# Kernel optimization log

Measured on AMD Instinct MI355X. Metric: run time of the kernel, lower is better.

## Reference

```python
import jax, jax.numpy as jnp
import numpy as np

B, T, F = 2048, 128, 128
H, L, K = 512, 8, 10  # hidden_dim, levels, conv_size
CHUNK = H // L
GATES = 4 * H + 2 * L


def setup_inputs() -> dict:
    key = jax.random.key(0)
    ks = jax.random.split(key, 12)
    s_k = 1.0 / np.sqrt(F + 1)
    s_r = 1.0 / np.sqrt(H + 1)
    s_s = 1.0 / np.sqrt(H)
    s_rs = 1.0 / np.sqrt(H // 6)
    s_c = 1.0 / np.sqrt(H * K)
    return {
        'x': jax.random.normal(ks[0], (B, T, F), jnp.float32),
        'time': jax.random.uniform(ks[1], (B, T), jnp.float32),
        'Wk': jax.random.normal(ks[2], (F + 1, GATES), jnp.float32) * s_k,
        'bk': jnp.zeros((GATES,), jnp.float32),
        'Wr': jax.random.normal(ks[3], (H + 1, GATES), jnp.float32) * s_r,
        'br': jnp.zeros((GATES,), jnp.float32),
        'Ws': jax.random.normal(ks[4], (H, H // 6), jnp.float32) * s_s,
        'bs': jax.random.normal(ks[5], (H // 6,), jnp.float32) * 0.01,
        'Wrs': jax.random.normal(ks[6], (H // 6, H), jnp.float32) * s_rs,
        'brs': jax.random.normal(ks[7], (H,), jnp.float32) * 0.01,
        'conv_w': jax.random.normal(ks[8], (H, H, K), jnp.float32) * s_c,  # [out_ch, in_ch, k]
        'conv_b': jax.random.normal(ks[9], (H,), jnp.float32) * 0.01,
    }


def _cumax_l2r(z):
    return jnp.cumsum(jax.nn.softmax(z, axis=-1), axis=-1)


def _cumax_r2l(z):
    return jnp.flip(jnp.cumsum(jax.nn.softmax(jnp.flip(z, -1), axis=-1), axis=-1), -1)


def _phase_forward(x, time, Wk, bk, Wr, br, Ws, bs, Wrs, brs, conv_w, conv_b):
    def step(carry, xs):
        c, h, tmp_h, tmp_dis = carry
        xt, dt = xs
        dt = dt[:, None]
        xo = (jnp.concatenate([xt, dt], -1) @ Wk + bk
              + jnp.concatenate([h, dt], -1) @ Wr + br)  # [B, 4H+2L]
        fm = _cumax_l2r(xo[:, :L])[:, :, None]        # [B, L, 1]
        im = _cumax_r2l(xo[:, L:2 * L])[:, :, None]   # [B, L, 1]
        g = xo[:, 2 * L:].reshape(-1, 4 * L, CHUNK)
        f = jax.nn.sigmoid(g[:, :L])
        i = jax.nn.sigmoid(g[:, L:2 * L])
        o = jax.nn.sigmoid(g[:, 2 * L:3 * L])
        c_in = jnp.tanh(g[:, 3 * L:])
        c_last = c.reshape(-1, L, CHUNK)
        ov = fm * im
        c_new = ov * (f * c_last + i * c_in) + (fm - ov) * c_last + (im - ov) * c_in
        h_new = (o * jnp.tanh(c_new)).reshape(-1, H)
        dist = 1.0 - jnp.mean(fm[..., 0], axis=-1)   # [B]
        tmp_h = jnp.concatenate([tmp_h[1:], h_new[None]], 0)
        tmp_dis = jnp.concatenate([tmp_dis[1:], dist[None]], 0)
        return (c_new.reshape(-1, H), h_new, tmp_h, tmp_dis), dist

    init = (jnp.zeros((B, H), x.dtype), jnp.zeros((B, H), x.dtype),
            jnp.zeros((K, B, H), x.dtype), jnp.zeros((K, B), x.dtype))
    (_, _, tmp_h, tmp_dis), distance = jax.lax.scan(
        step, init, (jnp.transpose(x, (1, 0, 2)), time.T))

    local_dis = jax.nn.softmax(jnp.cumsum(tmp_dis.T, axis=1), axis=1)   # [B, K]
    local_h = jnp.transpose(tmp_h, (1, 2, 0)) * local_dis[:, None, :]   # [B, H, K]
    theme = jax.nn.sigmoid(
        jnp.maximum(jnp.mean(local_h, axis=-1) @ Ws + bs, 0.0) @ Wrs + brs)  # [B, H]
    conv_out = jnp.einsum('bhk,ohk->bo', local_h, conv_w) + conv_b      # valid conv, out len 1
    return theme * conv_out, distance


def reference(x, time, Wk, bk, Wr, br, Ws, bs, Wrs, brs, conv_w, conv_b):
    return _phase_forward(x, time, Wk, bk, Wr, br, Ws, bs, Wrs, brs, conv_w, conv_b)
```

## Files before the change

### kernel.cpp

```cpp
#include <hip/hip_runtime.h>
#include <hip/hip_bf16.h>
#include <cstddef>
#include <cstdint>

namespace {

constexpr int B = 2048, T = 128, F = 128, H = 512, L = 8, KW = 10;
constexpr int GATES = 2064;
constexpr int NG = 2048;
constexpr int KIN = 640;
constexpr int HS = 85;
constexpr int RC = H * KW;
constexpr int KS = 8;
constexpr int NROW = 144;

constexpr int ABUF = 0;
constexpr int BRES = 16384;
constexpr int BROT = 126976;
constexpr int DTSO = 154624;
constexpr int SMEM_SZ = 155136;

typedef __attribute__((ext_vector_type(8))) short short8;
typedef __attribute__((ext_vector_type(4))) float f32x4;
typedef unsigned long long ull;

__device__ __forceinline__ float fsigmoid_(float x) {
    return __builtin_amdgcn_rcpf(1.0f + __expf(-x));
}
__device__ __forceinline__ float ftanh_(float x) {
    return 1.0f - 2.0f * __builtin_amdgcn_rcpf(1.0f + __expf(2.0f * x));
}

__device__ __forceinline__ void gl_lds16(const void* g, void* l) {
    __builtin_amdgcn_global_load_lds(
        (const __attribute__((address_space(1))) unsigned int*)g,
        (__attribute__((address_space(3))) unsigned int*)l,
        16, 0, 0);
}

__device__ __forceinline__ ull h_atomic_load(const void* p) {
    return __hip_atomic_load((const ull*)p, __ATOMIC_RELAXED, __HIP_MEMORY_SCOPE_AGENT);
}

__global__ __launch_bounds__(256) void prep_wgt(
    const float* __restrict__ Wk, const float* __restrict__ Wr,
    __hip_bfloat16* __restrict__ WgT)
{
    __shared__ float tile[64 * 65];
    const int tid = threadIdx.x;
    const int c0 = blockIdx.x * 64, k0 = blockIdx.y * 64;
#pragma unroll
    for (int rep = 0; rep < 16; ++rep) {
        int e = rep * 256 + tid;
        int kl = e >> 6, cl = e & 63;
        int col = c0 + cl;
        int nt = col >> 7, cc = col & 127;
        int n = 16 + ((cc >> 4) & 3) * 512 + nt * 32 + ((cc >> 6) & 1) * 16 + (cc & 15);
        int k = k0 + kl;
        tile[kl * 65 + cl] = (k < F) ? Wk[(size_t)k * GATES + n] : Wr[(size_t)(k - F) * GATES + n];
    }
    __syncthreads();
    const int cl = tid >> 2, q = tid & 3;
    unsigned short buf[16];
#pragma unroll
    for (int i = 0; i < 16; ++i) {
        float f = tile[(q * 16 + i) * 65 + cl];
        __hip_bfloat16 bv = __float2bfloat16(f);
        buf[i] = *(unsigned short*)&bv;
    }
    int col = c0 + cl;
    int nt = col >> 7, rin = col & 127;
    unsigned short* dst = (unsigned short*)WgT + (size_t)nt * NROW * KIN + (size_t)rin * KIN + k0 + q * 16;
    *(short8*)dst = *(short8*)&buf[0];
    *(short8*)(dst + 8) = *(short8*)&buf[8];
}

__global__ void prep_w16rep(const float* __restrict__ Wk, const float* __restrict__ Wr,
                            __hip_bfloat16* __restrict__ WgT)
{
    int idx = blockIdx.x * blockDim.x + threadIdx.x;
    if (idx >= 16 * 16 * KIN) return;
    int nt = idx / (16 * KIN);
    int rem = idx % (16 * KIN);
    int n = rem / KIN, k = rem % KIN;
    float v = (k < F) ? Wk[(size_t)k * GATES + n] : Wr[(size_t)(k - F) * GATES + n];
    WgT[(size_t)nt * NROW * KIN + (size_t)(128 + n) * KIN + k] = __float2bfloat16(v);
}

__global__ void prep_small(const float* __restrict__ Wk, const float* __restrict__ bk,
                           const float* __restrict__ Wr, const float* __restrict__ br,
                           float* __restrict__ biasg, float* __restrict__ wrowg,
                           float* __restrict__ bias16, float* __restrict__ wrow16)
{
    const int total = 2 * NG + 32;
    for (int idx = threadIdx.x; idx < total; idx += 256) {
        if (idx < NG) {
            int col = idx;
            int nt = col >> 7, cc = col & 127;
            int n = 16 + ((cc >> 4) & 3) * 512 + nt * 32 + ((cc >> 6) & 1) * 16 + (cc & 15);
            biasg[col] = bk[n] + br[n];
        } else if (idx < 2 * NG) {
            int col = idx - NG;
            int nt = col >> 7, cc = col & 127;
            int n = 16 + ((cc >> 4) & 3) * 512 + nt * 32 + ((cc >> 6) & 1) * 16 + (cc & 15);
            wrowg[col] = Wk[(size_t)F * GATES + n] + Wr[(size_t)H * GATES + n];
        } else if (idx < 2 * NG + 16) {
            int n = idx - 2 * NG;
            bias16[n] = bk[n] + br[n];
        } else {
            int n = idx - 2 * NG - 16;
            wrow16[n] = Wk[(size_t)F * GATES + n] + Wr[(size_t)H * GATES + n];
        }
    }
}

__global__ void convert_x(const float* __restrict__ x, __hip_bfloat16* __restrict__ xb) {
    int i = blockIdx.x * blockDim.x + threadIdx.x;
    size_t o = (size_t)i * 4;
    if (o >= (size_t)B * T * F) return;
    float4 v = *(const float4*)(x + o);
    xb[o + 0] = __float2bfloat16(v.x);
    xb[o + 1] = __float2bfloat16(v.y);
    xb[o + 2] = __float2bfloat16(v.z);
    xb[o + 3] = __float2bfloat16(v.w);
}

__global__ void prep_convw(const float* __restrict__ conv_w, __hip_bfloat16* __restrict__ CWb) {
    int i = blockIdx.x * blockDim.x + threadIdx.x;
    if (i >= H * RC / 4) return;
    size_t o = (size_t)i * 4;
    float4 v = *(const float4*)(conv_w + o);
    CWb[o + 0] = __float2bfloat16(v.x);
    CWb[o + 1] = __float2bfloat16(v.y);
    CWb[o + 2] = __float2bfloat16(v.z);
    CWb[o + 3] = __float2bfloat16(v.w);
}

__global__ __launch_bounds__(256) void prep_tmet(const float* __restrict__ tin,
                                                 float* __restrict__ tout)
{
    __shared__ float tl[32][33];
    const int bb = blockIdx.x * 32, tt = blockIdx.y * 32;
    const int tx = threadIdx.x & 31, ty = threadIdx.x >> 5;
#pragma unroll
    for (int r = 0; r < 32; r += 8)
        tl[ty + r][tx] = tin[(size_t)(bb + ty + r) * T + tt + tx];
    __syncthreads();
#pragma unroll
    for (int r = 0; r < 32; r += 8)
        tout[(size_t)(tt + ty + r) * B + bb + tx] = tl[tx][ty + r];
}

struct StepArgs {
    const __hip_bfloat16* xb;
    __hip_bfloat16* h0;
    __hip_bfloat16* h1;
    const __hip_bfloat16* WgT;
    const float* biasg;
    const float* wrowg;
    const float* bias16;
    const float* wrow16;
    const float* tmeT;
    __hip_bfloat16* tmp_h;
    float* tmp_ds;
    float* dist_out;
    unsigned* bar;
};

__global__ __launch_bounds__(512, 2) void persistent_step(StepArgs a)
{
    __shared__ __align__(16) char smem[SMEM_SZ];
    float* logitS = (float*)smem;
    float* fmimS = (float*)(smem + BROT);
    unsigned short* hstageS = (unsigned short*)(smem + 135168);
    float* dts = (float*)(smem + DTSO);

    const int tid = threadIdx.x;
    const int wave = tid >> 6;
    const int wr = wave >> 1, wc = wave & 1;
    const int quad = (tid & 63) >> 4, m16 = tid & 15;
    const int l = blockIdx.x;
    const int nt = ((l & 7) << 1) | ((l >> 3) & 1);
    const int mt = l >> 4;
    const int m0 = mt * 128;

    const int o0 = tid * 16;
    const int arow = o0 >> 6;
    const int asl = ((((o0 >> 4) & 3) ^ ((arow >> 1) & 3)) << 3);
    const char* xbT = (const char*)a.xb + (size_t)(m0 + arow) * (T * F * 2) + asl * 2;
    const size_t hbyte = (size_t)(m0 + arow) * (H * 2) + asl * 2;
    const unsigned short* wgt_tile = (const unsigned short*)a.WgT + (size_t)nt * NROW * KIN;
    const int brow0 = o0 >> 6;
    const int bsl0 = ((((o0 >> 4) & 3) ^ ((brow0 >> 1) & 3)) << 3);
    const char* bsT0 = (const char*)(wgt_tile + (size_t)brow0 * KIN + bsl0);
    const int ob1 = 8192 + tid * 16;
    const int brow1 = ob1 >> 6;
    const int bsl1 = ((((ob1 >> 4) & 3) ^ ((brow1 >> 1) & 3)) << 3);
    const char* bsT1 = (const char*)(wgt_tile + (size_t)brow1 * KIN + bsl1);
    const bool bv1 = (tid < 64);

    auto stageB = [&](int s, int bufbyte) {
        gl_lds16(bsT0 + s * 64, smem + bufbyte + o0);
        if (bv1) gl_lds16(bsT1 + s * 64, smem + bufbyte + ob1);
    };

    const int hcol = nt * 32 + wc * 16 + m16;
    const int lidx = hcol >> 6;
    float bj[4], wj[4];
#pragma unroll
    for (int j = 0; j < 4; ++j) {
        int col = nt * 128 + wc * 64 + j * 16 + m16;
        bj[j] = a.biasg[col];
        wj[j] = a.wrowg[col];
    }
    float b16r[16], w16r[16];
#pragma unroll
    for (int n = 0; n < 16; ++n) { b16r[n] = a.bias16[n]; w16r[n] = a.wrow16[n]; }

    const unsigned short* Abase = (const unsigned short*)smem;

    float creg[2][4] = {};
    ull areg[2][2];

    {
#pragma unroll
        for (int s = 0; s < 12; ++s) stageB(s, BRES + s * 9216);
        gl_lds16(xbT, smem + o0);
        stageB(12, BROT + 0 * 9216);
        stageB(13, BROT + 1 * 9216);
        areg[1][0] = h_atomic_load(xbT + 64);  areg[1][1] = h_atomic_load(xbT + 72);
        areg[0][0] = h_atomic_load(xbT + 128); areg[0][1] = h_atomic_load(xbT + 136);
    }
    __syncthreads();

#pragma unroll 1
    for (int t = 0; t < T; ++t) {
        const char* xt = xbT + (size_t)t * 256;
        const char* hs = (const char*)((t & 1) ? a.h1 : a.h0) + hbyte;
        unsigned* hout32 = (unsigned*)((t & 1) ? a.h0 : a.h1);

        if (tid < 128) dts[tid] = a.tmeT[(size_t)t * B + m0 + tid];

        f32x4 acc[2][4] = {};
        f32x4 acc16[2] = {};

#pragma unroll
        for (int ki = 0; ki < 20; ++ki) {
            if (ki > 0) {
                if (ki <= 13) {
                    asm volatile("s_waitcnt lgkmcnt(0)" ::: "memory");
                } else if (ki <= 17) {
                    if (bv1) asm volatile("s_waitcnt vmcnt(6) lgkmcnt(0)" ::: "memory");
                    else     asm volatile("s_waitcnt vmcnt(5) lgkmcnt(0)" ::: "memory");
                } else if (ki == 18) {
                    if (bv1) asm volatile("s_waitcnt vmcnt(4) lgkmcnt(0)" ::: "memory");
                    else     asm volatile("s_waitcnt vmcnt(3) lgkmcnt(0)" ::: "memory");
                } else {
                    asm volatile("s_waitcnt vmcnt(0) lgkmcnt(0)" ::: "memory");
                }
                __builtin_amdgcn_s_barrier();
                __builtin_amdgcn_sched_barrier(0);
            }
            const int nxt = ki + 1;
            if (nxt < 20) {
                char* adst = smem + (nxt & 1) * 8192 + o0;
                *(ull*)adst = areg[nxt & 1][0];
                *(ull*)(adst + 8) = areg[nxt & 1][1];
            }
            if (ki >= 12 && ki <= 17) {
                const int s = ki + 2;
                stageB(s, BROT + ((s - 12) % 3) * 9216);
            }
            __builtin_amdgcn_sched_barrier(0);
            const int fut = ki + 3;
            if (fut < 20) {
                if (fut <= 3) {
                    areg[fut & 1][0] = h_atomic_load(xt + fut * 64);
                    areg[fut & 1][1] = h_atomic_load(xt + fut * 64 + 8);
                } else {
                    areg[fut & 1][0] = h_atomic_load(hs + fut * 64 - 256);
                    areg[fut & 1][1] = h_atomic_load(hs + fut * 64 - 248);
                }
            }
            __builtin_amdgcn_sched_barrier(0);
            const unsigned short* A = Abase + (ki & 1) * 4096;
            const unsigned short* Bb = (const unsigned short*)
                (smem + (ki < 12 ? BRES + ki * 9216 : BROT + ((ki - 12) % 3) * 9216));
            short8 av[2], bv[4];
#pragma unroll
            for (int i = 0; i < 2; ++i) {
                int ar = wr * 32 + i * 16 + m16;
                av[i] = *(const short8*)&A[ar * 32 + ((quad ^ ((ar >> 1) & 3)) << 3)];
            }
#pragma unroll
            for (int j = 0; j < 4; ++j) {
                int br = wc * 64 + j * 16 + m16;
                bv[j] = *(const short8*)&Bb[br * 32 + ((quad ^ ((br >> 1) & 3)) << 3)];
            }
#pragma unroll
            for (int i = 0; i < 2; ++i)
#pragma unroll
                for (int j = 0; j < 4; ++j)
                    acc[i][j] = __builtin_amdgcn_mfma_f32_16x16x32_bf16(av[i], bv[j], acc[i][j], 0, 0, 0);
            if (wc == 0) {
                int lr = 128 + m16;
                short8 wv = *(const short8*)&Bb[lr * 32 + ((quad ^ ((lr >> 1) & 3)) << 3)];
                acc16[0] = __builtin_amdgcn_mfma_f32_16x16x32_bf16(av[0], wv, acc16[0], 0, 0, 0);
                acc16[1] = __builtin_amdgcn_mfma_f32_16x16x32_bf16(av[1], wv, acc16[1], 0, 0, 0);
            }
        }
        __syncthreads();

        if (wc == 0) {
#pragma unroll
            for (int i = 0; i < 2; ++i)
#pragma unroll
                for (int r = 0; r < 4; ++r)
                    logitS[(wr * 32 + i * 16 + quad * 4 + r) * 17 + m16] = acc16[i][r];
        }
        __syncthreads();

        if (tid < 256) {
            const int row = tid & 127;
            const int m = m0 + row;
            const bool hi = tid >= 128;
            const float dt = dts[row];
            const int off = hi ? 8 : 0;
            float z[8];
#pragma unroll
            for (int n = 0; n < 8; ++n)
                z[n] = logitS[row * 17 + off + n] + b16r[off + n] + dt * w16r[off + n];
            float mx = z[0];
#pragma unroll
            for (int j = 1; j < 8; ++j) mx = fmaxf(mx, z[j]);
            float e[8], s = 0.f;
#pragma unroll
            for (int j = 0; j < 8; ++j) { e[j] = __expf(z[j] - mx); s += e[j]; }
            const float inv = __builtin_amdgcn_rcpf(s);
            if (!hi) {
                float run = 0.f, fsum = 0.f;
#pragma unroll
                for (int j = 0; j < 8; ++j) { run += e[j]; float fmv = run * inv; fmimS[row * 16 + j] = fmv; fsum += fmv; }
                if (nt == 0) {
                    float d = 1.0f - fsum * 0.125f;
                    a.dist_out[(size_t)t * B + m] = d;
                    if (t >= T - KW) a.tmp_ds[(size_t)(t - (T - KW)) * B + m] = d;
                }
            } else {
                float run = 0.f;
#pragma unroll
                for (int j = 7; j >= 0; --j) { run += e[j]; fmimS[row * 16 + 8 + j] = run * inv; }
            }
        }
        __syncthreads();

#pragma unroll
        for (int i = 0; i < 2; ++i) {
#pragma unroll
            for (int r = 0; r < 4; ++r) {
                int rl = wr * 32 + i * 16 + quad * 4 + r;
                int m = m0 + rl;
                float dt = dts[rl];
                float fmv = fmimS[rl * 16 + lidx];
                float imv = fmimS[rl * 16 + 8 + lidx];
                float fg = fsigmoid_(acc[i][0][r] + bj[0] + dt * wj[0]);
                float ig = fsigmoid_(acc[i][1][r] + bj[1] + dt * wj[1]);
                float og = fsigmoid_(acc[i][2][r] + bj[2] + dt * wj[2]);
                float ci = ftanh_(acc[i][3][r] + bj[3] + dt * wj[3]);
                float ov = fmv * imv;
                float cl = creg[i][r];
                float cn = ov * (fg * cl + ig * ci) + (fmv - ov) * cl + (imv - ov) * ci;
                float hn = og * ftanh_(cn);
                creg[i][r] = cn;
                __hip_bfloat16 hb = __float2bfloat16(hn);
                hstageS[rl * 32 + (wc * 16 + m16)] = *(unsigned short*)&hb;
                if (t >= T - KW) a.tmp_h[((size_t)(t - (T - KW)) * B + m) * H + hcol] = hb;
            }
        }
        __syncthreads();

        {
            const unsigned* hs32 = (const unsigned*)hstageS;
#pragma unroll
            for (int wds = 0; wds < 4; ++wds) {
                int wi = wds * 512 + tid;
                int row = wi >> 4, cp = wi & 15;
                unsigned v = hs32[row * 16 + cp];
                __hip_atomic_store(hout32 + (size_t)(m0 + row) * (H / 2) + nt * 16 + cp, v,
                                   __ATOMIC_RELAXED, __HIP_MEMORY_SCOPE_AGENT);
            }
        }

        __syncthreads();
        if (t != T - 1) {
            const char* xn = xbT + (size_t)(t + 1) * 256;
            gl_lds16(xn, smem + o0);
            stageB(12, BROT + 0 * 9216);
            stageB(13, BROT + 1 * 9216);
            areg[1][0] = h_atomic_load(xn + 64);  areg[1][1] = h_atomic_load(xn + 72);
            areg[0][0] = h_atomic_load(xn + 128); areg[0][1] = h_atomic_load(xn + 136);
            if (tid == 0) {
                unsigned* ctr = a.bar + (mt << 6);
                __hip_atomic_fetch_add(ctr, 1u, __ATOMIC_RELAXED, __HIP_MEMORY_SCOPE_AGENT);
                const unsigned tgt = 16u * (unsigned)(t + 1);
                for (int it = 0; it < (1 << 22); ++it) {
                    if (__hip_atomic_load(ctr, __ATOMIC_RELAXED, __HIP_MEMORY_SCOPE_AGENT) >= tgt) break;
                    __builtin_amdgcn_s_sleep(2);
                }
            }
            __syncthreads();
        }
    }
}

__global__ __launch_bounds__(128) void post_local(
    const __hip_bfloat16* __restrict__ tmp_h, const float* __restrict__ tmp_dis,
    float* __restrict__ mean_h, __hip_bfloat16* __restrict__ Ahk)
{
    const int b = blockIdx.x;
    const int tid = threadIdx.x;
    __shared__ float ld[KW];
    if (tid == 0) {
        float cd[KW];
        float run = 0.f;
        for (int k = 0; k < KW; ++k) { run += tmp_dis[(size_t)k * B + b]; cd[k] = run; }
        float mx = cd[0];
        for (int k = 1; k < KW; ++k) mx = fmaxf(mx, cd[k]);
        float s = 0.f;
        for (int k = 0; k < KW; ++k) { cd[k] = expf(cd[k] - mx); s += cd[k]; }
        for (int k = 0; k < KW; ++k) ld[k] = cd[k] / s;
    }
    __syncthreads();
    float ldr[KW];
#pragma unroll
    for (int k = 0; k < KW; ++k) ldr[k] = ld[k];
    for (int h = tid; h < H; h += 128) {
        float s = 0.f;
#pragma unroll
        for (int k = 0; k < KW; ++k) {
            float v = __bfloat162float(tmp_h[((size_t)k * B + b) * H + h]) * ldr[k];
            s += v;
            Ahk[(size_t)b * RC + h * KW + k] = __float2bfloat16(v);
        }
        mean_h[(size_t)b * H + h] = s * (1.0f / KW);
    }
}

__global__ void theme1_k(const float* __restrict__ mean_h, const float* __restrict__ Ws,
                         const float* __restrict__ bs, float* __restrict__ t1)
{
    int idx = blockIdx.x * blockDim.x + threadIdx.x;
    if (idx >= B * HS) return;
    int b = idx / HS, j = idx % HS;
    float s = bs[j];
    const float* mh = mean_h + (size_t)b * H;
    for (int h = 0; h < H; ++h) s += mh[h] * Ws[(size_t)h * HS + j];
    t1[idx] = fmaxf(s, 0.f);
}

__global__ void theme2_k(const float* __restrict__ t1, const float* __restrict__ Wrs,
                         const float* __restrict__ brs, float* __restrict__ theme)
{
    int idx = blockIdx.x * blockDim.x + threadIdx.x;
    if (idx >= B * H) return;
    int b = idx / H, o = idx % H;
    float s = brs[o];
    const float* tv = t1 + (size_t)b * HS;
    for (int j = 0; j < HS; ++j) s += tv[j] * Wrs[(size_t)j * H + o];
    theme[idx] = 1.0f / (1.0f + expf(-s));
}

__global__ __launch_bounds__(256) void conv_split(
    const __hip_bfloat16* __restrict__ Ahk, const __hip_bfloat16* __restrict__ CWb,
    float* __restrict__ Pbuf)
{
    __shared__ __align__(16) unsigned short As2[128 * 64];
    __shared__ __align__(16) unsigned short Bs2[128 * 64];
    const int tid = threadIdx.x;
    const int wave = tid >> 6;
    const int wr = wave >> 1, wc = wave & 1;
    const int quad = (tid & 63) >> 4, m16 = tid & 15;
    const int n0 = blockIdx.x * 128, m0 = blockIdx.y * 128;
    const int ksb = blockIdx.z * (RC / KS);

    f32x4 acc[4][4] = {};
    for (int k0 = 0; k0 < RC / KS; k0 += 64) {
#pragma unroll
        for (int p = 0; p < 4; ++p) {
            int o = p * 4096 + tid * 16;
            int row = o >> 7, slot = (o >> 4) & 7;
            int kg = ksb + k0 + (slot ^ (row & 7)) * 8;
            gl_lds16((const unsigned short*)Ahk + (size_t)(m0 + row) * RC + kg, (char*)As2 + o);
            gl_lds16((const unsigned short*)CWb + (size_t)(n0 + row) * RC + kg, (char*)Bs2 + o);
        }
        __syncthreads();
#pragma unroll
        for (int c2 = 0; c2 < 2; ++c2) {
            const int k8 = c2 * 4 + quad;
            short8 av[4], bv[4];
#pragma unroll
            for (int i = 0; i < 4; ++i) {
                int arow = wr * 64 + i * 16 + m16;
                av[i] = *(const short8*)&As2[arow * 64 + (k8 ^ (arow & 7)) * 8];
            }
#pragma unroll
            for (int j = 0; j < 4; ++j) {
                int brow = wc * 64 + j * 16 + m16;
                bv[j] = *(const short8*)&Bs2[brow * 64 + (k8 ^ (brow & 7)) * 8];
            }
#pragma unroll
            for (int i = 0; i < 4; ++i)
#pragma unroll
                for (int j = 0; j < 4; ++j)
                    acc[i][j] = __builtin_amdgcn_mfma_f32_16x16x32_bf16(av[i], bv[j], acc[i][j], 0, 0, 0);
        }
        __syncthreads();
    }
    float* P = Pbuf + (size_t)blockIdx.z * B * H;
#pragma unroll
    for (int j = 0; j < 4; ++j) {
        const int col = n0 + wc * 64 + j * 16 + m16;
#pragma unroll
        for (int i = 0; i < 4; ++i) {
            const int rb = m0 + wr * 64 + i * 16 + quad * 4;
#pragma unroll
            for (int r = 0; r < 4; ++r)
                P[(size_t)(rb + r) * H + col] = acc[i][j][r];
        }
    }
}

__global__ void conv_reduce(const float* __restrict__ Pbuf, const float* __restrict__ conv_b,
                            const float* __restrict__ theme, float* __restrict__ out0)
{
    int i = blockIdx.x * blockDim.x + threadIdx.x;
    if (i >= B * H) return;
    float s = conv_b[i & (H - 1)];
#pragma unroll
    for (int ks = 0; ks < KS; ++ks) s += Pbuf[(size_t)ks * B * H + i];
    out0[i] = theme[i] * s;
}

}

extern "C" void kernel_launch(void* const* d_in, const int* in_sizes, int n_in,
                              void* d_out, int out_size, void* d_ws, size_t ws_size,
                              hipStream_t stream)
{
    (void)in_sizes; (void)n_in; (void)out_size; (void)ws_size;
    const float* x      = (const float*)d_in[0];
    const float* tme    = (const float*)d_in[1];
    const float* Wk     = (const float*)d_in[2];
    const float* bk     = (const float*)d_in[3];
    const float* Wr     = (const float*)d_in[4];
    const float* br     = (const float*)d_in[5];
    const float* Ws     = (const float*)d_in[6];
    const float* bs     = (const float*)d_in[7];
    const float* Wrs    = (const float*)d_in[8];
    const float* brs    = (const float*)d_in[9];
    const float* conv_w = (const float*)d_in[10];
    const float* conv_b = (const float*)d_in[11];

    float* out0 = (float*)d_out;
    float* dist_out = out0 + (size_t)B * H;

    char* w = (char*)d_ws;
    __hip_bfloat16* WgT  = (__hip_bfloat16*)w; w += (size_t)16 * NROW * KIN * 2;
    __hip_bfloat16* xb   = (__hip_bfloat16*)w; w += (size_t)B * T * F * 2;
    __hip_bfloat16* CWb  = (__hip_bfloat16*)w; w += (size_t)H * RC * 2;
    __hip_bfloat16* Ahk  = (__hip_bfloat16*)w; w += (size_t)B * RC * 2;
    __hip_bfloat16* hb0  = (__hip_bfloat16*)w; w += (size_t)B * H * 2;
    __hip_bfloat16* hb1  = (__hip_bfloat16*)w; w += (size_t)B * H * 2;
    __hip_bfloat16* tmp_h = (__hip_bfloat16*)w; w += (size_t)KW * B * H * 2;
    float* biasg  = (float*)w; w += (size_t)NG * 4;
    float* wrowg  = (float*)w; w += (size_t)NG * 4;
    float* bias16 = (float*)w; w += 64;
    float* wrow16 = (float*)w; w += 64;
    float* tmp_ds = (float*)w; w += (size_t)KW * B * 4;
    float* mean_h = (float*)w; w += (size_t)B * H * 4;
    float* t1     = (float*)w; w += (size_t)B * HS * 4;
    float* theme  = (float*)w; w += (size_t)B * H * 4;
    float* Pbuf   = (float*)w; w += (size_t)KS * B * H * 4;
    float* tmeT   = (float*)w; w += (size_t)T * B * 4;
    unsigned* bar = (unsigned*)w; w += 4096;

    hipMemsetAsync(hb0, 0, (size_t)B * H * sizeof(__hip_bfloat16), stream);
    hipMemsetAsync(bar, 0, 4096, stream);

    prep_wgt<<<dim3(NG / 64, KIN / 64), 256, 0, stream>>>(Wk, Wr, WgT);
    prep_w16rep<<<(16 * 16 * KIN + 255) / 256, 256, 0, stream>>>(Wk, Wr, WgT);
    prep_small<<<1, 256, 0, stream>>>(Wk, bk, Wr, br, biasg, wrowg, bias16, wrow16);
    convert_x<<<((B * T * F / 4) + 255) / 256, 256, 0, stream>>>(x, xb);
    prep_convw<<<((H * RC / 4) + 255) / 256, 256, 0, stream>>>(conv_w, CWb);
    prep_tmet<<<dim3(B / 32, T / 32), 256, 0, stream>>>(tme, tmeT);

    {
        StepArgs sa;
        sa.xb = xb; sa.h0 = hb0; sa.h1 = hb1; sa.WgT = WgT;
        sa.biasg = biasg; sa.wrowg = wrowg; sa.bias16 = bias16; sa.wrow16 = wrow16;
        sa.tmeT = tmeT; sa.tmp_h = tmp_h; sa.tmp_ds = tmp_ds; sa.dist_out = dist_out;
        sa.bar = bar;
        persistent_step<<<256, 512, 0, stream>>>(sa);
    }

    post_local<<<B, 128, 0, stream>>>(tmp_h, tmp_ds, mean_h, Ahk);
    theme1_k<<<(B * HS + 255) / 256, 256, 0, stream>>>(mean_h, Ws, bs, t1);
    theme2_k<<<(B * H + 255) / 256, 256, 0, stream>>>(t1, Wrs, brs, theme);
    conv_split<<<dim3(H / 128, B / 128, KS), 256, 0, stream>>>(Ahk, CWb, Pbuf);
    conv_reduce<<<(B * H + 255) / 256, 256, 0, stream>>>(Pbuf, conv_b, theme, out0);
}
```

Baseline: 1.771 ms.

## Load A fragments directly into registers and keep 18 B slices resident in LDS

```diff
diff --git a/kernel.cpp b/kernel.cpp
--- a/kernel.cpp
+++ b/kernel.cpp
@@ -14,11 +14,15 @@
 constexpr int KS = 8;
 constexpr int NROW = 144;
 
-constexpr int ABUF = 0;
-constexpr int BRES = 16384;
-constexpr int BROT = 126976;
-constexpr int DTSO = 154624;
-constexpr int SMEM_SZ = 155136;
+constexpr int BSLICE = 8192;
+constexpr int NRES = 18;
+constexpr int RINGA = 147456;
+constexpr int RINGB = 155648;
+constexpr int LOGO  = 147456;
+constexpr int HSTO  = 147456;
+constexpr int DTSO2 = 156160;
+constexpr int FMIMO = 156672;
+constexpr int SMEM_SZ = 163840;
 
 typedef __attribute__((ext_vector_type(8))) short short8;
 typedef __attribute__((ext_vector_type(4))) float f32x4;
@@ -170,10 +174,10 @@
 __global__ __launch_bounds__(512, 2) void persistent_step(StepArgs a)
 {
     __shared__ __align__(16) char smem[SMEM_SZ];
-    float* logitS = (float*)smem;
-    float* fmimS = (float*)(smem + BROT);
-    unsigned short* hstageS = (unsigned short*)(smem + 135168);
-    float* dts = (float*)(smem + DTSO);
+    float* logitS = (float*)(smem + LOGO);
+    float* fmimS  = (float*)(smem + FMIMO);
+    unsigned short* hstageS = (unsigned short*)(smem + HSTO);
+    float* dts = (float*)(smem + DTSO2);
 
     const int tid = threadIdx.x;
     const int wave = tid >> 6;
@@ -183,29 +187,34 @@
     const int nt = ((l & 7) << 1) | ((l >> 3) & 1);
     const int mt = l >> 4;
     const int m0 = mt * 128;
+    const int lidx = nt >> 1;
 
     const int o0 = tid * 16;
-    const int arow = o0 >> 6;
-    const int asl = ((((o0 >> 4) & 3) ^ ((arow >> 1) & 3)) << 3);
-    const char* xbT = (const char*)a.xb + (size_t)(m0 + arow) * (T * F * 2) + asl * 2;
-    const size_t hbyte = (size_t)(m0 + arow) * (H * 2) + asl * 2;
-    const unsigned short* wgt_tile = (const unsigned short*)a.WgT + (size_t)nt * NROW * KIN;
     const int brow0 = o0 >> 6;
     const int bsl0 = ((((o0 >> 4) & 3) ^ ((brow0 >> 1) & 3)) << 3);
+    const unsigned short* wgt_tile = (const unsigned short*)a.WgT + (size_t)nt * NROW * KIN;
     const char* bsT0 = (const char*)(wgt_tile + (size_t)brow0 * KIN + bsl0);
-    const int ob1 = 8192 + tid * 16;
-    const int brow1 = ob1 >> 6;
-    const int bsl1 = ((((ob1 >> 4) & 3) ^ ((brow1 >> 1) & 3)) << 3);
-    const char* bsT1 = (const char*)(wgt_tile + (size_t)brow1 * KIN + bsl1);
-    const bool bv1 = (tid < 64);
-
-    auto stageB = [&](int s, int bufbyte) {
-        gl_lds16(bsT0 + s * 64, smem + bufbyte + o0);
-        if (bv1) gl_lds16(bsT1 + s * 64, smem + bufbyte + ob1);
+    auto stageB = [&](int s, int off) {
+        gl_lds16(bsT0 + s * 64, smem + off + o0);
     };
 
+    const int arow0 = m0 + wr * 32 + m16;
+    const char* xA0 = (const char*)a.xb + (size_t)arow0 * (T * F * 2) + quad * 16;
+    const char* xA1 = xA0 + (size_t)16 * (T * F * 2);
+    const size_t hA0 = (size_t)arow0 * (H * 2) + quad * 16;
+    const size_t hA1 = hA0 + (size_t)16 * (H * 2);
+
+    ull wv20[20][2];
+    if (wc == 0) {
+        const unsigned short* lrow = wgt_tile + (size_t)(128 + m16) * KIN + quad * 8;
+#pragma unroll
+        for (int s = 0; s < 20; ++s) {
+            wv20[s][0] = *(const ull*)(lrow + s * 32);
+            wv20[s][1] = *(const ull*)(lrow + s * 32 + 4);
+        }
+    }
+
     const int hcol = nt * 32 + wc * 16 + m16;
-    const int lidx = hcol >> 6;
     float bj[4], wj[4];
 #pragma unroll
     for (int j = 0; j < 4; ++j) {
@@ -213,104 +222,83 @@
         bj[j] = a.biasg[col];
         wj[j] = a.wrowg[col];
     }
-    float b16r[16], w16r[16];
-#pragma unroll
-    for (int n = 0; n < 16; ++n) { b16r[n] = a.bias16[n]; w16r[n] = a.wrow16[n]; }
-
-    const unsigned short* Abase = (const unsigned short*)smem;
+    const int soff = (tid >= 128 && tid < 256) ? 8 : 0;
+    float b16r8[8], w16r8[8];
+#pragma unroll
+    for (int n = 0; n < 8; ++n) { b16r8[n] = a.bias16[soff + n]; w16r8[n] = a.wrow16[soff + n]; }
 
     float creg[2][4] = {};
-    ull areg[2][2];
+    ull af[3][2][2];
 
     {
 #pragma unroll
-        for (int s = 0; s < 12; ++s) stageB(s, BRES + s * 9216);
-        gl_lds16(xbT, smem + o0);
-        stageB(12, BROT + 0 * 9216);
-        stageB(13, BROT + 1 * 9216);
-        areg[1][0] = h_atomic_load(xbT + 64);  areg[1][1] = h_atomic_load(xbT + 72);
-        areg[0][0] = h_atomic_load(xbT + 128); areg[0][1] = h_atomic_load(xbT + 136);
+        for (int s = 0; s < NRES; ++s) stageB(s, s * BSLICE);
+        stageB(18, RINGA);
+        stageB(19, RINGB);
+        af[0][0][0] = *(const ull*)(xA0);      af[0][0][1] = *(const ull*)(xA0 + 8);
+        af[0][1][0] = *(const ull*)(xA1);      af[0][1][1] = *(const ull*)(xA1 + 8);
+        af[1][0][0] = *(const ull*)(xA0 + 64); af[1][0][1] = *(const ull*)(xA0 + 72);
+        af[1][1][0] = *(const ull*)(xA1 + 64); af[1][1][1] = *(const ull*)(xA1 + 72);
     }
     __syncthreads();
 
 #pragma unroll 1
     for (int t = 0; t < T; ++t) {
-        const char* xt = xbT + (size_t)t * 256;
-        const char* hs = (const char*)((t & 1) ? a.h1 : a.h0) + hbyte;
+        const char* xt0 = xA0 + (size_t)t * 256;
+        const char* xt1 = xA1 + (size_t)t * 256;
+        const char* hbuf = (const char*)((t & 1) ? a.h1 : a.h0);
         unsigned* hout32 = (unsigned*)((t & 1) ? a.h0 : a.h1);
 
-        if (tid < 128) dts[tid] = a.tmeT[(size_t)t * B + m0 + tid];
+        float dtreg = 0.f;
+        if (tid < 128) dtreg = a.tmeT[(size_t)t * B + m0 + tid];
 
         f32x4 acc[2][4] = {};
         f32x4 acc16[2] = {};
 
 #pragma unroll
         for (int ki = 0; ki < 20; ++ki) {
-            if (ki > 0) {
-                if (ki <= 13) {
-                    asm volatile("s_waitcnt lgkmcnt(0)" ::: "memory");
-                } else if (ki <= 17) {
-                    if (bv1) asm volatile("s_waitcnt vmcnt(6) lgkmcnt(0)" ::: "memory");
-                    else     asm volatile("s_waitcnt vmcnt(5) lgkmcnt(0)" ::: "memory");
-                } else if (ki == 18) {
-                    if (bv1) asm volatile("s_waitcnt vmcnt(4) lgkmcnt(0)" ::: "memory");
-                    else     asm volatile("s_waitcnt vmcnt(3) lgkmcnt(0)" ::: "memory");
+            const int ld = ki + 2;
+            if (ld < 20) {
+                const int slot = ld % 3;
+                if (ld <= 3) {
+                    af[slot][0][0] = *(const ull*)(xt0 + ld * 64);
+                    af[slot][0][1] = *(const ull*)(xt0 + ld * 64 + 8);
+                    af[slot][1][0] = *(const ull*)(xt1 + ld * 64);
+                    af[slot][1][1] = *(const ull*)(xt1 + ld * 64 + 8);
                 } else {
-                    asm volatile("s_waitcnt vmcnt(0) lgkmcnt(0)" ::: "memory");
+                    const size_t ko = (size_t)ld * 64 - 256;
+                    af[slot][0][0] = h_atomic_load(hbuf + hA0 + ko);
+                    af[slot][0][1] = h_atomic_load(hbuf + hA0 + ko + 8);
+                    af[slot][1][0] = h_atomic_load(hbuf + hA1 + ko);
+                    af[slot][1][1] = h_atomic_load(hbuf + hA1 + ko + 8);
                 }
-                __builtin_amdgcn_s_barrier();
-                __builtin_amdgcn_sched_barrier(0);
-            }
-            const int nxt = ki + 1;
-            if (nxt < 20) {
-                char* adst = smem + (nxt & 1) * 8192 + o0;
-                *(ull*)adst = areg[nxt & 1][0];
-                *(ull*)(adst + 8) = areg[nxt & 1][1];
-            }
-            if (ki >= 12 && ki <= 17) {
-                const int s = ki + 2;
-                stageB(s, BROT + ((s - 12) % 3) * 9216);
-            }
-            __builtin_amdgcn_sched_barrier(0);
-            const int fut = ki + 3;
-            if (fut < 20) {
-                if (fut <= 3) {
-                    areg[fut & 1][0] = h_atomic_load(xt + fut * 64);
-                    areg[fut & 1][1] = h_atomic_load(xt + fut * 64 + 8);
-                } else {
-                    areg[fut & 1][0] = h_atomic_load(hs + fut * 64 - 256);
-                    areg[fut & 1][1] = h_atomic_load(hs + fut * 64 - 248);
-                }
-            }
-            __builtin_amdgcn_sched_barrier(0);
-            const unsigned short* A = Abase + (ki & 1) * 4096;
-            const unsigned short* Bb = (const unsigned short*)
-                (smem + (ki < 12 ? BRES + ki * 9216 : BROT + ((ki - 12) % 3) * 9216));
-            short8 av[2], bv[4];
-#pragma unroll
-            for (int i = 0; i < 2; ++i) {
-                int ar = wr * 32 + i * 16 + m16;
-                av[i] = *(const short8*)&A[ar * 32 + ((quad ^ ((ar >> 1) & 3)) << 3)];
-            }
+            }
+            const unsigned short* Bb = (const unsigned short*)(smem +
+                (ki < NRES ? ki * BSLICE : (ki == 18 ? RINGA : RINGB)));
+            short8 bvv[4];
 #pragma unroll
             for (int j = 0; j < 4; ++j) {
                 int br = wc * 64 + j * 16 + m16;
-                bv[j] = *(const short8*)&Bb[br * 32 + ((quad ^ ((br >> 1) & 3)) << 3)];
-            }
-#pragma unroll
-            for (int i = 0; i < 2; ++i)
-#pragma unroll
-                for (int j = 0; j < 4; ++j)
-                    acc[i][j] = __builtin_amdgcn_mfma_f32_16x16x32_bf16(av[i], bv[j], acc[i][j], 0, 0, 0);
+                bvv[j] = *(const short8*)&Bb[br * 32 + ((quad ^ ((br >> 1) & 3)) << 3)];
+            }
+            short8 av0, av1;
+            ((ull*)&av0)[0] = af[ki % 3][0][0]; ((ull*)&av0)[1] = af[ki % 3][0][1];
+            ((ull*)&av1)[0] = af[ki % 3][1][0]; ((ull*)&av1)[1] = af[ki % 3][1][1];
+#pragma unroll
+            for (int j = 0; j < 4; ++j) {
+                acc[0][j] = __builtin_amdgcn_mfma_f32_16x16x32_bf16(av0, bvv[j], acc[0][j], 0, 0, 0);
+                acc[1][j] = __builtin_amdgcn_mfma_f32_16x16x32_bf16(av1, bvv[j], acc[1][j], 0, 0, 0);
+            }
             if (wc == 0) {
-                int lr = 128 + m16;
-                short8 wv = *(const short8*)&Bb[lr * 32 + ((quad ^ ((lr >> 1) & 3)) << 3)];
-                acc16[0] = __builtin_amdgcn_mfma_f32_16x16x32_bf16(av[0], wv, acc16[0], 0, 0, 0);
-                acc16[1] = __builtin_amdgcn_mfma_f32_16x16x32_bf16(av[1], wv, acc16[1], 0, 0, 0);
+                short8 wv;
+                ((ull*)&wv)[0] = wv20[ki][0]; ((ull*)&wv)[1] = wv20[ki][1];
+                acc16[0] = __builtin_amdgcn_mfma_f32_16x16x32_bf16(av0, wv, acc16[0], 0, 0, 0);
+                acc16[1] = __builtin_amdgcn_mfma_f32_16x16x32_bf16(av1, wv, acc16[1], 0, 0, 0);
             }
         }
         __syncthreads();
 
+        if (tid < 128) dts[tid] = dtreg;
         if (wc == 0) {
 #pragma unroll
             for (int i = 0; i < 2; ++i)
@@ -324,12 +312,11 @@
             const int row = tid & 127;
             const int m = m0 + row;
             const bool hi = tid >= 128;
-            const float dt = dts[row];
-            const int off = hi ? 8 : 0;
+            const float dt = hi ? dts[row] : dtreg;
             float z[8];
 #pragma unroll
             for (int n = 0; n < 8; ++n)
-                z[n] = logitS[row * 17 + off + n] + b16r[off + n] + dt * w16r[off + n];
+                z[n] = logitS[row * 17 + soff + n] + b16r8[n] + dt * w16r8[n];
             float mx = z[0];
 #pragma unroll
             for (int j = 1; j < 8; ++j) mx = fmaxf(mx, z[j]);
@@ -338,18 +325,28 @@
             for (int j = 0; j < 8; ++j) { e[j] = __expf(z[j] - mx); s += e[j]; }
             const float inv = __builtin_amdgcn_rcpf(s);
             if (!hi) {
-                float run = 0.f, fsum = 0.f;
-#pragma unroll
-                for (int j = 0; j < 8; ++j) { run += e[j]; float fmv = run * inv; fmimS[row * 16 + j] = fmv; fsum += fmv; }
+                float run = 0.f, fsum = 0.f, val = 0.f;
+#pragma unroll
+                for (int j = 0; j < 8; ++j) {
+                    run += e[j];
+                    float fmv = run * inv;
+                    if (j == lidx) val = fmv;
+                    fsum += fmv;
+                }
+                fmimS[row * 2] = val;
                 if (nt == 0) {
                     float d = 1.0f - fsum * 0.125f;
                     a.dist_out[(size_t)t * B + m] = d;
                     if (t >= T - KW) a.tmp_ds[(size_t)(t - (T - KW)) * B + m] = d;
                 }
             } else {
-                float run = 0.f;
-#pragma unroll
-                for (int j = 7; j >= 0; --j) { run += e[j]; fmimS[row * 16 + 8 + j] = run * inv; }
+                float run = 0.f, val = 0.f;
+#pragma unroll
+                for (int j = 7; j >= 0; --j) {
+                    run += e[j];
+                    if (j == lidx) val = run * inv;
+                }
+                fmimS[row * 2 + 1] = val;
             }
         }
         __syncthreads();
@@ -361,8 +358,8 @@
                 int rl = wr * 32 + i * 16 + quad * 4 + r;
                 int m = m0 + rl;
                 float dt = dts[rl];
-                float fmv = fmimS[rl * 16 + lidx];
-                float imv = fmimS[rl * 16 + 8 + lidx];
+                float fmv = fmimS[rl * 2];
+                float imv = fmimS[rl * 2 + 1];
                 float fg = fsigmoid_(acc[i][0][r] + bj[0] + dt * wj[0]);
                 float ig = fsigmoid_(acc[i][1][r] + bj[1] + dt * wj[1]);
                 float og = fsigmoid_(acc[i][2][r] + bj[2] + dt * wj[2]);
@@ -393,12 +390,14 @@
 
         __syncthreads();
         if (t != T - 1) {
-            const char* xn = xbT + (size_t)(t + 1) * 256;
-            gl_lds16(xn, smem + o0);
-            stageB(12, BROT + 0 * 9216);
-            stageB(13, BROT + 1 * 9216);
-            areg[1][0] = h_atomic_load(xn + 64);  areg[1][1] = h_atomic_load(xn + 72);
-            areg[0][0] = h_atomic_load(xn + 128); areg[0][1] = h_atomic_load(xn + 136);
+            const char* xn0 = xA0 + (size_t)(t + 1) * 256;
+            const char* xn1 = xA1 + (size_t)(t + 1) * 256;
+            stageB(18, RINGA);
+            stageB(19, RINGB);
+            af[0][0][0] = *(const ull*)(xn0);      af[0][0][1] = *(const ull*)(xn0 + 8);
+            af[0][1][0] = *(const ull*)(xn1);      af[0][1][1] = *(const ull*)(xn1 + 8);
+            af[1][0][0] = *(const ull*)(xn0 + 64); af[1][0][1] = *(const ull*)(xn0 + 72);
+            af[1][1][0] = *(const ull*)(xn1 + 64); af[1][1][1] = *(const ull*)(xn1 + 72);
             if (tid == 0) {
                 unsigned* ctr = a.bar + (mt << 6);
                 __hip_atomic_fetch_add(ctr, 1u, __ATOMIC_RELAXED, __HIP_MEMORY_SCOPE_AGENT);
```

Measured after the change: 3.230 ms. +82.4%, slower.

## Keep ladder weight rows in registers and enlarge resident LDS weight slices

Applied to the files above, without the earlier changes.

```diff
diff --git a/kernel.cpp b/kernel.cpp
--- a/kernel.cpp
+++ b/kernel.cpp
@@ -14,11 +14,15 @@
 constexpr int KS = 8;
 constexpr int NROW = 144;
 
+constexpr int BSLICE = 8192;
 constexpr int ABUF = 0;
 constexpr int BRES = 16384;
-constexpr int BROT = 126976;
-constexpr int DTSO = 154624;
-constexpr int SMEM_SZ = 155136;
+constexpr int BRING = 139264;
+constexpr int LOGO  = 139264;
+constexpr int DTSO  = 147968;
+constexpr int FMIMO = 148480;
+constexpr int HSTO  = 149504;
+constexpr int SMEM_SZ = 163840;
 
 typedef __attribute__((ext_vector_type(8))) short short8;
 typedef __attribute__((ext_vector_type(4))) float f32x4;
@@ -170,9 +174,9 @@
 __global__ __launch_bounds__(512, 2) void persistent_step(StepArgs a)
 {
     __shared__ __align__(16) char smem[SMEM_SZ];
-    float* logitS = (float*)smem;
-    float* fmimS = (float*)(smem + BROT);
-    unsigned short* hstageS = (unsigned short*)(smem + 135168);
+    float* logitS = (float*)(smem + LOGO);
+    float* fmimS  = (float*)(smem + FMIMO);
+    unsigned short* hstageS = (unsigned short*)(smem + HSTO);
     float* dts = (float*)(smem + DTSO);
 
     const int tid = threadIdx.x;
@@ -183,6 +187,7 @@
     const int nt = ((l & 7) << 1) | ((l >> 3) & 1);
     const int mt = l >> 4;
     const int m0 = mt * 128;
+    const int lidx = nt >> 1;
 
     const int o0 = tid * 16;
     const int arow = o0 >> 6;
@@ -190,22 +195,22 @@
     const char* xbT = (const char*)a.xb + (size_t)(m0 + arow) * (T * F * 2) + asl * 2;
     const size_t hbyte = (size_t)(m0 + arow) * (H * 2) + asl * 2;
     const unsigned short* wgt_tile = (const unsigned short*)a.WgT + (size_t)nt * NROW * KIN;
-    const int brow0 = o0 >> 6;
-    const int bsl0 = ((((o0 >> 4) & 3) ^ ((brow0 >> 1) & 3)) << 3);
-    const char* bsT0 = (const char*)(wgt_tile + (size_t)brow0 * KIN + bsl0);
-    const int ob1 = 8192 + tid * 16;
-    const int brow1 = ob1 >> 6;
-    const int bsl1 = ((((ob1 >> 4) & 3) ^ ((brow1 >> 1) & 3)) << 3);
-    const char* bsT1 = (const char*)(wgt_tile + (size_t)brow1 * KIN + bsl1);
-    const bool bv1 = (tid < 64);
-
-    auto stageB = [&](int s, int bufbyte) {
-        gl_lds16(bsT0 + s * 64, smem + bufbyte + o0);
-        if (bv1) gl_lds16(bsT1 + s * 64, smem + bufbyte + ob1);
+    const char* bsT0 = (const char*)(wgt_tile + (size_t)arow * KIN + asl);
+    auto stageB = [&](int s, int off) {
+        gl_lds16(bsT0 + s * 64, smem + off + o0);
     };
 
+    ull wv20[20][2];
+    if (wc == 0) {
+        const unsigned short* lrow = wgt_tile + (size_t)(128 + m16) * KIN + quad * 8;
+#pragma unroll
+        for (int s = 0; s < 20; ++s) {
+            wv20[s][0] = *(const ull*)(lrow + s * 32);
+            wv20[s][1] = *(const ull*)(lrow + s * 32 + 4);
+        }
+    }
+
     const int hcol = nt * 32 + wc * 16 + m16;
-    const int lidx = hcol >> 6;
     float bj[4], wj[4];
 #pragma unroll
     for (int j = 0; j < 4; ++j) {
@@ -213,9 +218,10 @@
         bj[j] = a.biasg[col];
         wj[j] = a.wrowg[col];
     }
-    float b16r[16], w16r[16];
-#pragma unroll
-    for (int n = 0; n < 16; ++n) { b16r[n] = a.bias16[n]; w16r[n] = a.wrow16[n]; }
+    const int soff = (tid >= 128 && tid < 256) ? 8 : 0;
+    float b16r8[8], w16r8[8];
+#pragma unroll
+    for (int n = 0; n < 8; ++n) { b16r8[n] = a.bias16[soff + n]; w16r8[n] = a.wrow16[soff + n]; }
 
     const unsigned short* Abase = (const unsigned short*)smem;
 
@@ -224,12 +230,10 @@
 
     {
 #pragma unroll
-        for (int s = 0; s < 12; ++s) stageB(s, BRES + s * 9216);
+        for (int s = 0; s < 15; ++s) stageB(s, BRES + s * BSLICE);
         gl_lds16(xbT, smem + o0);
-        stageB(12, BROT + 0 * 9216);
-        stageB(13, BROT + 1 * 9216);
-        areg[1][0] = h_atomic_load(xbT + 64);  areg[1][1] = h_atomic_load(xbT + 72);
-        areg[0][0] = h_atomic_load(xbT + 128); areg[0][1] = h_atomic_load(xbT + 136);
+        areg[1][0] = *(const ull*)(xbT + 64);  areg[1][1] = *(const ull*)(xbT + 72);
+        areg[0][0] = *(const ull*)(xbT + 128); areg[0][1] = *(const ull*)(xbT + 136);
     }
     __syncthreads();
 
@@ -239,7 +243,8 @@
         const char* hs = (const char*)((t & 1) ? a.h1 : a.h0) + hbyte;
         unsigned* hout32 = (unsigned*)((t & 1) ? a.h0 : a.h1);
 
-        if (tid < 128) dts[tid] = a.tmeT[(size_t)t * B + m0 + tid];
+        float dtreg = 0.f;
+        if (tid < 128) dtreg = a.tmeT[(size_t)t * B + m0 + tid];
 
         f32x4 acc[2][4] = {};
         f32x4 acc16[2] = {};
@@ -247,17 +252,14 @@
 #pragma unroll
         for (int ki = 0; ki < 20; ++ki) {
             if (ki > 0) {
-                if (ki <= 13) {
+                if (ki <= 14)
                     asm volatile("s_waitcnt lgkmcnt(0)" ::: "memory");
-                } else if (ki <= 17) {
-                    if (bv1) asm volatile("s_waitcnt vmcnt(6) lgkmcnt(0)" ::: "memory");
-                    else     asm volatile("s_waitcnt vmcnt(5) lgkmcnt(0)" ::: "memory");
-                } else if (ki == 18) {
-                    if (bv1) asm volatile("s_waitcnt vmcnt(4) lgkmcnt(0)" ::: "memory");
-                    else     asm volatile("s_waitcnt vmcnt(3) lgkmcnt(0)" ::: "memory");
-                } else {
+                else if (ki <= 17)
+                    asm volatile("s_waitcnt vmcnt(5) lgkmcnt(0)" ::: "memory");
+                else if (ki == 18)
+                    asm volatile("s_waitcnt vmcnt(3) lgkmcnt(0)" ::: "memory");
+                else
                     asm volatile("s_waitcnt vmcnt(0) lgkmcnt(0)" ::: "memory");
-                }
                 __builtin_amdgcn_s_barrier();
                 __builtin_amdgcn_sched_barrier(0);
             }
@@ -267,16 +269,15 @@
                 *(ull*)adst = areg[nxt & 1][0];
                 *(ull*)(adst + 8) = areg[nxt & 1][1];
             }
-            if (ki >= 12 && ki <= 17) {
-                const int s = ki + 2;
-                stageB(s, BROT + ((s - 12) % 3) * 9216);
+            if (ki >= 13 && ki <= 17) {
+                stageB(ki + 2, BRING + ((ki - 13) % 3) * BSLICE);
             }
             __builtin_amdgcn_sched_barrier(0);
             const int fut = ki + 3;
             if (fut < 20) {
                 if (fut <= 3) {
-                    areg[fut & 1][0] = h_atomic_load(xt + fut * 64);
-                    areg[fut & 1][1] = h_atomic_load(xt + fut * 64 + 8);
+                    areg[fut & 1][0] = *(const ull*)(xt + fut * 64);
+                    areg[fut & 1][1] = *(const ull*)(xt + fut * 64 + 8);
                 } else {
                     areg[fut & 1][0] = h_atomic_load(hs + fut * 64 - 256);
                     areg[fut & 1][1] = h_atomic_load(hs + fut * 64 - 248);
@@ -284,8 +285,8 @@
             }
             __builtin_amdgcn_sched_barrier(0);
             const unsigned short* A = Abase + (ki & 1) * 4096;
-            const unsigned short* Bb = (const unsigned short*)
-                (smem + (ki < 12 ? BRES + ki * 9216 : BROT + ((ki - 12) % 3) * 9216));
+            const unsigned short* Bb = (const unsigned short*)(smem +
+                (ki < 15 ? BRES + ki * BSLICE : BRING + ((ki - 15) % 3) * BSLICE));
             short8 av[2], bv[4];
 #pragma unroll
             for (int i = 0; i < 2; ++i) {
@@ -303,14 +304,15 @@
                 for (int j = 0; j < 4; ++j)
                     acc[i][j] = __builtin_amdgcn_mfma_f32_16x16x32_bf16(av[i], bv[j], acc[i][j], 0, 0, 0);
             if (wc == 0) {
-                int lr = 128 + m16;
-                short8 wv = *(const short8*)&Bb[lr * 32 + ((quad ^ ((lr >> 1) & 3)) << 3)];
+                short8 wv;
+                ((ull*)&wv)[0] = wv20[ki][0]; ((ull*)&wv)[1] = wv20[ki][1];
                 acc16[0] = __builtin_amdgcn_mfma_f32_16x16x32_bf16(av[0], wv, acc16[0], 0, 0, 0);
                 acc16[1] = __builtin_amdgcn_mfma_f32_16x16x32_bf16(av[1], wv, acc16[1], 0, 0, 0);
             }
         }
         __syncthreads();
 
+        if (tid < 128) dts[tid] = dtreg;
         if (wc == 0) {
 #pragma unroll
             for (int i = 0; i < 2; ++i)
@@ -324,12 +326,11 @@
             const int row = tid & 127;
             const int m = m0 + row;
             const bool hi = tid >= 128;
-            const float dt = dts[row];
-            const int off = hi ? 8 : 0;
+            const float dt = hi ? dts[row] : dtreg;
             float z[8];
 #pragma unroll
             for (int n = 0; n < 8; ++n)
-                z[n] = logitS[row * 17 + off + n] + b16r[off + n] + dt * w16r[off + n];
+                z[n] = logitS[row * 17 + soff + n] + b16r8[n] + dt * w16r8[n];
             float mx = z[0];
 #pragma unroll
             for (int j = 1; j < 8; ++j) mx = fmaxf(mx, z[j]);
@@ -338,18 +339,28 @@
             for (int j = 0; j < 8; ++j) { e[j] = __expf(z[j] - mx); s += e[j]; }
             const float inv = __builtin_amdgcn_rcpf(s);
             if (!hi) {
-                float run = 0.f, fsum = 0.f;
-#pragma unroll
-                for (int j = 0; j < 8; ++j) { run += e[j]; float fmv = run * inv; fmimS[row * 16 + j] = fmv; fsum += fmv; }
+                float run = 0.f, fsum = 0.f, val = 0.f;
+#pragma unroll
+                for (int j = 0; j < 8; ++j) {
+                    run += e[j];
+                    float fmv = run * inv;
+                    if (j == lidx) val = fmv;
+                    fsum += fmv;
+                }
+                fmimS[row * 2] = val;
                 if (nt == 0) {
                     float d = 1.0f - fsum * 0.125f;
                     a.dist_out[(size_t)t * B + m] = d;
                     if (t >= T - KW) a.tmp_ds[(size_t)(t - (T - KW)) * B + m] = d;
                 }
             } else {
-                float run = 0.f;
-#pragma unroll
-                for (int j = 7; j >= 0; --j) { run += e[j]; fmimS[row * 16 + 8 + j] = run * inv; }
+                float run = 0.f, val = 0.f;
+#pragma unroll
+                for (int j = 7; j >= 0; --j) {
+                    run += e[j];
+                    if (j == lidx) val = run * inv;
+                }
+                fmimS[row * 2 + 1] = val;
             }
         }
         __syncthreads();
@@ -361,8 +372,8 @@
                 int rl = wr * 32 + i * 16 + quad * 4 + r;
                 int m = m0 + rl;
                 float dt = dts[rl];
-                float fmv = fmimS[rl * 16 + lidx];
-                float imv = fmimS[rl * 16 + 8 + lidx];
+                float fmv = fmimS[rl * 2];
+                float imv = fmimS[rl * 2 + 1];
                 float fg = fsigmoid_(acc[i][0][r] + bj[0] + dt * wj[0]);
                 float ig = fsigmoid_(acc[i][1][r] + bj[1] + dt * wj[1]);
                 float og = fsigmoid_(acc[i][2][r] + bj[2] + dt * wj[2]);
@@ -395,10 +406,8 @@
         if (t != T - 1) {
             const char* xn = xbT + (size_t)(t + 1) * 256;
             gl_lds16(xn, smem + o0);
-            stageB(12, BROT + 0 * 9216);
-            stageB(13, BROT + 1 * 9216);
-            areg[1][0] = h_atomic_load(xn + 64);  areg[1][1] = h_atomic_load(xn + 72);
-            areg[0][0] = h_atomic_load(xn + 128); areg[0][1] = h_atomic_load(xn + 136);
+            areg[1][0] = *(const ull*)(xn + 64);  areg[1][1] = *(const ull*)(xn + 72);
+            areg[0][0] = *(const ull*)(xn + 128); areg[0][1] = *(const ull*)(xn + 136);
             if (tid == 0) {
                 unsigned* ctr = a.bar + (mt << 6);
                 __hip_atomic_fetch_add(ctr, 1u, __ATOMIC_RELAXED, __HIP_MEMORY_SCOPE_AGENT);
@@ -500,8 +509,8 @@
             short8 av[4], bv[4];
 #pragma unroll
             for (int i = 0; i < 4; ++i) {
-                int arow = wr * 64 + i * 16 + m16;
-                av[i] = *(const short8*)&As2[arow * 64 + (k8 ^ (arow & 7)) * 8];
+                int arow2 = wr * 64 + i * 16 + m16;
+                av[i] = *(const short8*)&As2[arow2 * 64 + (k8 ^ (arow2 & 7)) * 8];
             }
 #pragma unroll
             for (int j = 0; j < 4; ++j) {
```

Result: slower. 2.354 ms (+32.9%).
